# Kernel tuning notes

Hardware: AMD Instinct MI355X
Metric: run time of the kernel (lower is better)

## Reference

```python
import jax, jax.numpy as jnp
import numpy as np

B, QN, KN, DIN, DPROJ = 8, 2048, 2048, 1024, 1024

def setup_inputs() -> dict:
    key = jax.random.key(0)
    ks = jax.random.split(key, 10)
    s = 1.0 / np.sqrt(DIN)
    return {
        "query": jax.random.normal(ks[0], (B, QN, DIN), jnp.float32),
        "key": jax.random.normal(ks[1], (B, KN, DIN), jnp.float32),
        "value": jax.random.normal(ks[2], (B, KN, DIN), jnp.float32),
        "mask": jax.random.randint(ks[3], (B, KN), 0, 2, jnp.int32),
        "Wq": jax.random.uniform(ks[4], (DPROJ, DIN), jnp.float32, -s, s),
        "bq": jax.random.uniform(ks[5], (DPROJ,), jnp.float32, -s, s),
        "Wk": jax.random.uniform(ks[6], (DPROJ, DIN), jnp.float32, -s, s),
        "bk": jax.random.uniform(ks[7], (DPROJ,), jnp.float32, -s, s),
        "Wv": jax.random.uniform(ks[8], (DPROJ, DIN), jnp.float32, -s, s),
        "bv": jax.random.uniform(ks[9], (DPROJ,), jnp.float32, -s, s),
    }

def reference(query, key, value, mask, Wq, bq, Wk, bk, Wv, bv):
    pq = jnp.einsum('bqc,dc->bqd', query, Wq) + bq  # (b, qn, dproj)
    pk = jnp.einsum('bkc,dc->bkd', key, Wk) + bk    # (b, kn, dproj)
    pv = jnp.einsum('bkc,dc->bkd', value, Wv) + bv  # (b, kn, dproj)
    scores = jnp.einsum('bqd,bkd->bqk', pq, pk) / jnp.sqrt(jnp.float32(DPROJ))
    m = mask[:, None, :]  # (b, 1, kn) broadcasts over qn
    scores = jnp.where(m == 0, jnp.float32(-1e9), scores)
    attn = jax.nn.softmax(scores, axis=-1)
    attn = attn * m.astype(attn.dtype)  # post-softmax double mask
    ctx = jnp.einsum('bqk,bkd->bqd', attn, pv)
    return (ctx, attn)
```

## Files before the change

### kernel.cpp

```cpp
#include <hip/hip_runtime.h>
#include <hip/hip_bf16.h>


typedef __bf16 bf16;
typedef __bf16 bf16x4 __attribute__((ext_vector_type(4)));
typedef __bf16 bf16x8 __attribute__((ext_vector_type(8)));
typedef float f32x4 __attribute__((ext_vector_type(4)));

#define TILE 128
#define BK 32

__device__ __forceinline__ void gld_lds16(const bf16* g, bf16* l) {
  __builtin_amdgcn_global_load_lds(
      (const __attribute__((address_space(1))) void*)g,
      (__attribute__((address_space(3))) void*)l, 16, 0, 0);
}

__global__ __launch_bounds__(256, 2)
void gemm_f32in(const float* __restrict__ A, int lda,
                const float* __restrict__ Bt, int ldb,
                bf16* __restrict__ C, int ldc,
                const float* __restrict__ bias, int bias_mode, int K)
{
  __shared__ bf16 As[TILE * BK];
  __shared__ bf16 Bs[TILE * BK];
  const int tid = threadIdx.x;
  const int wave = tid >> 6, lane = tid & 63;
  const int wm = (wave >> 1) * 64, wn = (wave & 1) * 64;
  const long m0 = (long)blockIdx.x * TILE;
  const long n0 = (long)blockIdx.y * TILE;

  f32x4 acc[4][4] = {};
  const int fr = lane & 15, fq = lane >> 4;

  for (int k0 = 0; k0 < K; k0 += BK) {
    __syncthreads();
#pragma unroll
    for (int j = 0; j < 4; ++j) {
      int c = j * 256 + tid;
      int row = c >> 3, col = (c & 7) * 4;
      f32x4 av = *(const f32x4*)&A[(m0 + row) * (long)lda + k0 + col];
      f32x4 bv = *(const f32x4*)&Bt[(n0 + row) * (long)ldb + k0 + col];
      bf16x4 ab, bb;
      ab[0] = (bf16)av[0]; ab[1] = (bf16)av[1]; ab[2] = (bf16)av[2]; ab[3] = (bf16)av[3];
      bb[0] = (bf16)bv[0]; bb[1] = (bf16)bv[1]; bb[2] = (bf16)bv[2]; bb[3] = (bf16)bv[3];
      *(bf16x4*)&As[row * BK + col] = ab;
      *(bf16x4*)&Bs[row * BK + col] = bb;
    }
    __syncthreads();

    bf16x8 af[4], bg[4];
#pragma unroll
    for (int i = 0; i < 4; ++i)
      af[i] = *(const bf16x8*)&As[(wm + i * 16 + fr) * BK + fq * 8];
#pragma unroll
    for (int i = 0; i < 4; ++i)
      bg[i] = *(const bf16x8*)&Bs[(wn + i * 16 + fr) * BK + fq * 8];
#pragma unroll
    for (int mi = 0; mi < 4; ++mi)
#pragma unroll
      for (int ni = 0; ni < 4; ++ni)
        acc[mi][ni] = __builtin_amdgcn_mfma_f32_16x16x32_bf16(
            af[mi], bg[ni], acc[mi][ni], 0, 0, 0);
  }

  const int cc = lane & 15, cq = lane >> 4;
#pragma unroll
  for (int mi = 0; mi < 4; ++mi)
#pragma unroll
    for (int ni = 0; ni < 4; ++ni)
#pragma unroll
      for (int r = 0; r < 4; ++r) {
        int row = wm + mi * 16 + cq * 4 + r;
        int col = wn + ni * 16 + cc;
        float v = acc[mi][ni][r];
        if (bias_mode == 1) v += bias[n0 + col];
        else if (bias_mode == 2) v += bias[m0 + row];
        C[(m0 + row) * (long)ldc + (n0 + col)] = (bf16)v;
      }
}

__global__ __launch_bounds__(256, 2)
void gemm_bf16(const bf16* __restrict__ A, int lda, long sA,
               const bf16* __restrict__ Bt, int ldb, long sB,
               float* __restrict__ C, int ldc, long sC,
               int K, float scale)
{
  __shared__ bf16 As[TILE * BK];
  __shared__ bf16 Bs[TILE * BK];
  const int tid = threadIdx.x;
  const int wave = tid >> 6, lane = tid & 63;
  const int wm = (wave >> 1) * 64, wn = (wave & 1) * 64;
  const long m0 = (long)blockIdx.x * TILE;
  const long n0 = (long)blockIdx.y * TILE;
  A  += (long)blockIdx.z * sA;
  Bt += (long)blockIdx.z * sB;
  C  += (long)blockIdx.z * sC;

  f32x4 acc[4][4] = {};

  const int srow = tid >> 2;
  const int scol = (tid & 3) * 8;
  const bf16* Ag0 = A  + (m0 + srow) * (long)lda + scol;
  const bf16* Ag1 = A  + (m0 + 64 + srow) * (long)lda + scol;
  const bf16* Bg0 = Bt + (n0 + srow) * (long)ldb + scol;
  const bf16* Bg1 = Bt + (n0 + 64 + srow) * (long)ldb + scol;
  bf16* Al0 = &As[tid * 8];
  bf16* Al1 = &As[(256 + tid) * 8];
  bf16* Bl0 = &Bs[tid * 8];
  bf16* Bl1 = &Bs[(256 + tid) * 8];

  const int fr = lane & 15, fq = lane >> 4;

  for (int k0 = 0; k0 < K; k0 += BK) {
    __syncthreads();
    gld_lds16(Ag0 + k0, Al0);
    gld_lds16(Ag1 + k0, Al1);
    gld_lds16(Bg0 + k0, Bl0);
    gld_lds16(Bg1 + k0, Bl1);
    __syncthreads();

    bf16x8 af[4], bg[4];
#pragma unroll
    for (int i = 0; i < 4; ++i)
      af[i] = *(const bf16x8*)&As[(wm + i * 16 + fr) * BK + fq * 8];
#pragma unroll
    for (int i = 0; i < 4; ++i)
      bg[i] = *(const bf16x8*)&Bs[(wn + i * 16 + fr) * BK + fq * 8];
#pragma unroll
    for (int mi = 0; mi < 4; ++mi)
#pragma unroll
      for (int ni = 0; ni < 4; ++ni)
        acc[mi][ni] = __builtin_amdgcn_mfma_f32_16x16x32_bf16(
            af[mi], bg[ni], acc[mi][ni], 0, 0, 0);
  }

  const int cc = lane & 15, cq = lane >> 4;
#pragma unroll
  for (int mi = 0; mi < 4; ++mi)
#pragma unroll
    for (int ni = 0; ni < 4; ++ni)
#pragma unroll
      for (int r = 0; r < 4; ++r) {
        int row = wm + mi * 16 + cq * 4 + r;
        int col = wn + ni * 16 + cc;
        C[(m0 + row) * (long)ldc + (n0 + col)] = acc[mi][ni][r] * scale;
      }
}

__global__ __launch_bounds__(256)
void softmax_mask(const int* __restrict__ mask, float* __restrict__ attn,
                  bf16* __restrict__ attnb)
{
  const int row = blockIdx.x;
  const int b = row >> 11;
  float* arow = attn + (long)row * 2048;
  bf16* brow = attnb + (long)row * 2048;
  const int* mrow = mask + (b << 11);
  const int tid = threadIdx.x;
  const int lane = tid & 63, wave = tid >> 6;

  f32x4 s[2];
  int4 mk[2];
  s[0] = *(const f32x4*)&arow[tid * 4];
  s[1] = *(const f32x4*)&arow[1024 + tid * 4];
  mk[0] = *(const int4*)&mrow[tid * 4];
  mk[1] = *(const int4*)&mrow[1024 + tid * 4];
  const int m[8] = {mk[0].x, mk[0].y, mk[0].z, mk[0].w,
                    mk[1].x, mk[1].y, mk[1].z, mk[1].w};

  float mx = -3e38f;
#pragma unroll
  for (int i = 0; i < 8; ++i)
    if (m[i]) mx = fmaxf(mx, s[i >> 2][i & 3]);
#pragma unroll
  for (int off = 32; off > 0; off >>= 1) mx = fmaxf(mx, __shfl_xor(mx, off));
  __shared__ float rmax[4], rsum[4];
  if (lane == 0) rmax[wave] = mx;
  __syncthreads();
  mx = fmaxf(fmaxf(rmax[0], rmax[1]), fmaxf(rmax[2], rmax[3]));

  float e[8], sum = 0.f;
#pragma unroll
  for (int i = 0; i < 8; ++i) {
    e[i] = m[i] ? __expf(s[i >> 2][i & 3] - mx) : 0.f;
    sum += e[i];
  }
#pragma unroll
  for (int off = 32; off > 0; off >>= 1) sum += __shfl_xor(sum, off);
  if (lane == 0) rsum[wave] = sum;
  __syncthreads();
  sum = rsum[0] + rsum[1] + rsum[2] + rsum[3];
  float inv = sum > 0.f ? 1.f / sum : 0.f;

  f32x4 o; bf16x4 ob;
#pragma unroll
  for (int h = 0; h < 2; ++h) {
#pragma unroll
    for (int i = 0; i < 4; ++i) {
      float v = e[h * 4 + i] * inv;
      o[i] = v; ob[i] = (bf16)v;
    }
    *(f32x4*)&arow[h * 1024 + tid * 4] = o;
    *(bf16x4*)&brow[h * 1024 + tid * 4] = ob;
  }
}

extern "C" void kernel_launch(void* const* d_in, const int* in_sizes, int n_in,
                              void* d_out, int out_size, void* d_ws, size_t ws_size,
                              hipStream_t stream)
{
  const float* query = (const float*)d_in[0];
  const float* key   = (const float*)d_in[1];
  const float* value = (const float*)d_in[2];
  const int*   mask  = (const int*)d_in[3];
  const float* Wq = (const float*)d_in[4];
  const float* bq = (const float*)d_in[5];
  const float* Wk = (const float*)d_in[6];
  const float* bk = (const float*)d_in[7];
  const float* Wv = (const float*)d_in[8];
  const float* bv = (const float*)d_in[9];

  float* ctx  = (float*)d_out;
  float* attn = ctx + (size_t)8 * 2048 * 1024;

  bf16* Pq    = (bf16*)d_ws;
  bf16* Pk    = Pq + (size_t)16384 * 1024;
  bf16* PvT   = Pk + (size_t)16384 * 1024;
  bf16* attnb = (bf16*)d_ws;

  dim3 blk(256);

  hipLaunchKernelGGL(gemm_f32in, dim3(128, 8), blk, 0, stream,
      query, 1024, Wq, 1024, Pq, 1024, bq, 1, 1024);
  hipLaunchKernelGGL(gemm_f32in, dim3(128, 8), blk, 0, stream,
      key, 1024, Wk, 1024, Pk, 1024, bk, 1, 1024);
  hipLaunchKernelGGL(gemm_f32in, dim3(8, 128), blk, 0, stream,
      Wv, 1024, value, 1024, PvT, 16384, bv, 2, 1024);
  hipLaunchKernelGGL(gemm_bf16, dim3(16, 16, 8), blk, 0, stream,
      Pq, 1024, (long)2048 * 1024, Pk, 1024, (long)2048 * 1024,
      attn, 2048, (long)2048 * 2048, 1024, 0.03125f);
  hipLaunchKernelGGL(softmax_mask, dim3(16384), blk, 0, stream, mask, attn, attnb);
  hipLaunchKernelGGL(gemm_bf16, dim3(16, 8, 8), blk, 0, stream,
      attnb, 2048, (long)2048 * 2048, PvT, 16384, 2048L,
      ctx, 1024, (long)2048 * 1024, 2048, 1.0f);
}
```

Baseline: 766.0 us.

## Replace GEMMs with 256x256 8-wave pipelined kernel and pre-convert inputs to bf16

Adds a standalone f32-to-bf16 conversion pass for the inputs and weights, staged in the attn output buffer as scratch. All five GEMMs now use a new 512-thread kernel with 256x256 tiles, double-buffered LDS loaded through global_load_lds with XOR swizzle, split barriers and setprio. The score GEMM writes bf16 into the attn buffer, and softmax reads that bf16 data back, which halves score traffic at some cost in precision. The change brings more LDS use and extra conversion launches, and the intermediate scores now carry only bf16 precision.

```diff
diff --git a/kernel.cpp b/kernel.cpp
--- a/kernel.cpp
+++ b/kernel.cpp
@@ -7,8 +7,9 @@
 typedef __bf16 bf16x8 __attribute__((ext_vector_type(8)));
 typedef float f32x4 __attribute__((ext_vector_type(4)));
 
-#define TILE 128
-#define BK 32
+#define BAR() asm volatile("s_barrier" ::: "memory")
+#define WAIT_LGKM0() do { asm volatile("s_waitcnt lgkmcnt(0)" ::: "memory"); \
+                          __builtin_amdgcn_sched_barrier(0); } while (0)
 
 __device__ __forceinline__ void gld_lds16(const bf16* g, bf16* l) {
   __builtin_amdgcn_global_load_lds(
@@ -16,136 +17,201 @@
       (__attribute__((address_space(3))) void*)l, 16, 0, 0);
 }
 
-__global__ __launch_bounds__(256, 2)
-void gemm_f32in(const float* __restrict__ A, int lda,
-                const float* __restrict__ Bt, int ldb,
-                bf16* __restrict__ C, int ldc,
-                const float* __restrict__ bias, int bias_mode, int K)
+__global__ __launch_bounds__(256)
+void cvt_f32_bf16(const float* __restrict__ src, bf16* __restrict__ dst, int n)
 {
-  __shared__ bf16 As[TILE * BK];
-  __shared__ bf16 Bs[TILE * BK];
+  long i = ((long)blockIdx.x * 256 + threadIdx.x) * 8;
+  if (i >= n) return;
+  f32x4 a = *(const f32x4*)&src[i];
+  f32x4 b = *(const f32x4*)&src[i + 4];
+  bf16x8 o;
+  o[0] = (bf16)a[0]; o[1] = (bf16)a[1]; o[2] = (bf16)a[2]; o[3] = (bf16)a[3];
+  o[4] = (bf16)b[0]; o[5] = (bf16)b[1]; o[6] = (bf16)b[2]; o[7] = (bf16)b[3];
+  *(bf16x8*)&dst[i] = o;
+}
+
+__global__ __launch_bounds__(512, 2)
+void gemm8p(const bf16* __restrict__ A, int lda, long sA,
+            const bf16* __restrict__ Bt, int ldb, long sB,
+            void* __restrict__ Cout, int ldc, long sC, int c_bf16,
+            const float* __restrict__ bias, int bias_mode,
+            int K, float scale)
+{
+  extern __shared__ bf16 lds[];
   const int tid = threadIdx.x;
-  const int wave = tid >> 6, lane = tid & 63;
-  const int wm = (wave >> 1) * 64, wn = (wave & 1) * 64;
-  const long m0 = (long)blockIdx.x * TILE;
-  const long n0 = (long)blockIdx.y * TILE;
-
-  f32x4 acc[4][4] = {};
-  const int fr = lane & 15, fq = lane >> 4;
-
-  for (int k0 = 0; k0 < K; k0 += BK) {
-    __syncthreads();
-#pragma unroll
-    for (int j = 0; j < 4; ++j) {
-      int c = j * 256 + tid;
-      int row = c >> 3, col = (c & 7) * 4;
-      f32x4 av = *(const f32x4*)&A[(m0 + row) * (long)lda + k0 + col];
-      f32x4 bv = *(const f32x4*)&Bt[(n0 + row) * (long)ldb + k0 + col];
-      bf16x4 ab, bb;
-      ab[0] = (bf16)av[0]; ab[1] = (bf16)av[1]; ab[2] = (bf16)av[2]; ab[3] = (bf16)av[3];
-      bb[0] = (bf16)bv[0]; bb[1] = (bf16)bv[1]; bb[2] = (bf16)bv[2]; bb[3] = (bf16)bv[3];
-      *(bf16x4*)&As[row * BK + col] = ab;
-      *(bf16x4*)&Bs[row * BK + col] = bb;
-    }
-    __syncthreads();
-
-    bf16x8 af[4], bg[4];
-#pragma unroll
-    for (int i = 0; i < 4; ++i)
-      af[i] = *(const bf16x8*)&As[(wm + i * 16 + fr) * BK + fq * 8];
-#pragma unroll
-    for (int i = 0; i < 4; ++i)
-      bg[i] = *(const bf16x8*)&Bs[(wn + i * 16 + fr) * BK + fq * 8];
-#pragma unroll
-    for (int mi = 0; mi < 4; ++mi)
-#pragma unroll
-      for (int ni = 0; ni < 4; ++ni)
-        acc[mi][ni] = __builtin_amdgcn_mfma_f32_16x16x32_bf16(
-            af[mi], bg[ni], acc[mi][ni], 0, 0, 0);
-  }
-
-  const int cc = lane & 15, cq = lane >> 4;
-#pragma unroll
-  for (int mi = 0; mi < 4; ++mi)
-#pragma unroll
-    for (int ni = 0; ni < 4; ++ni)
-#pragma unroll
-      for (int r = 0; r < 4; ++r) {
-        int row = wm + mi * 16 + cq * 4 + r;
-        int col = wn + ni * 16 + cc;
-        float v = acc[mi][ni][r];
-        if (bias_mode == 1) v += bias[n0 + col];
-        else if (bias_mode == 2) v += bias[m0 + row];
-        C[(m0 + row) * (long)ldc + (n0 + col)] = (bf16)v;
-      }
-}
-
-__global__ __launch_bounds__(256, 2)
-void gemm_bf16(const bf16* __restrict__ A, int lda, long sA,
-               const bf16* __restrict__ Bt, int ldb, long sB,
-               float* __restrict__ C, int ldc, long sC,
-               int K, float scale)
-{
-  __shared__ bf16 As[TILE * BK];
-  __shared__ bf16 Bs[TILE * BK];
-  const int tid = threadIdx.x;
-  const int wave = tid >> 6, lane = tid & 63;
-  const int wm = (wave >> 1) * 64, wn = (wave & 1) * 64;
-  const long m0 = (long)blockIdx.x * TILE;
-  const long n0 = (long)blockIdx.y * TILE;
+  const int lane = tid & 63;
+  const int wid = tid >> 6;
+  const int wr = wid >> 2;
+  const int wc = wid & 3;
+  const long m0 = (long)blockIdx.x * 256;
+  const long n0 = (long)blockIdx.y * 256;
   A  += (long)blockIdx.z * sA;
   Bt += (long)blockIdx.z * sB;
-  C  += (long)blockIdx.z * sC;
-
-  f32x4 acc[4][4] = {};
-
-  const int srow = tid >> 2;
-  const int scol = (tid & 3) * 8;
-  const bf16* Ag0 = A  + (m0 + srow) * (long)lda + scol;
-  const bf16* Ag1 = A  + (m0 + 64 + srow) * (long)lda + scol;
-  const bf16* Bg0 = Bt + (n0 + srow) * (long)ldb + scol;
-  const bf16* Bg1 = Bt + (n0 + 64 + srow) * (long)ldb + scol;
-  bf16* Al0 = &As[tid * 8];
-  bf16* Al1 = &As[(256 + tid) * 8];
-  bf16* Bl0 = &Bs[tid * 8];
-  bf16* Bl1 = &Bs[(256 + tid) * 8];
 
   const int fr = lane & 15, fq = lane >> 4;
-
-  for (int k0 = 0; k0 < K; k0 += BK) {
-    __syncthreads();
-    gld_lds16(Ag0 + k0, Al0);
-    gld_lds16(Ag1 + k0, Al1);
-    gld_lds16(Bg0 + k0, Bl0);
-    gld_lds16(Bg1 + k0, Bl1);
-    __syncthreads();
-
-    bf16x8 af[4], bg[4];
-#pragma unroll
-    for (int i = 0; i < 4; ++i)
-      af[i] = *(const bf16x8*)&As[(wm + i * 16 + fr) * BK + fq * 8];
-#pragma unroll
-    for (int i = 0; i < 4; ++i)
-      bg[i] = *(const bf16x8*)&Bs[(wn + i * 16 + fr) * BK + fq * 8];
-#pragma unroll
-    for (int mi = 0; mi < 4; ++mi)
-#pragma unroll
-      for (int ni = 0; ni < 4; ++ni)
-        acc[mi][ni] = __builtin_amdgcn_mfma_f32_16x16x32_bf16(
-            af[mi], bg[ni], acc[mi][ni], 0, 0, 0);
+  const int cs0 = (((fq * 16)      ^ ((fr & 7) << 4)) >> 1);
+  const int cs1 = (((64 + fq * 16) ^ ((fr & 7) << 4)) >> 1);
+  const int rbA = (wr * 128 + fr) * 64;
+  const int rbB = 16384 + (wc * 64 + fr) * 64;
+
+  const int srow = tid >> 3;
+  const int slot = (tid & 7) ^ (srow & 7);
+  const bf16* Ag[4]; const bf16* Bg[4];
+#pragma unroll
+  for (int h = 0; h < 2; ++h)
+#pragma unroll
+    for (int i = 0; i < 2; ++i) {
+      Ag[h * 2 + i] = A  + (m0 + h * 128 + i * 64 + srow) * (long)lda + slot * 8;
+      Bg[h * 2 + i] = Bt + (n0 + h * 128 + i * 64 + srow) * (long)ldb + slot * 8;
+    }
+  const int ldst = tid * 8;
+
+  const int NT = K >> 6;
+  f32x4 acc[8][4] = {};
+
+#pragma unroll
+  for (int hi = 0; hi < 4; ++hi)
+    gld_lds16(Ag[hi], &lds[(hi >> 1) * 8192 + (hi & 1) * 4096 + ldst]);
+#pragma unroll
+  for (int hi = 0; hi < 4; ++hi)
+    gld_lds16(Bg[hi], &lds[16384 + (hi >> 1) * 8192 + (hi & 1) * 4096 + ldst]);
+#pragma unroll
+  for (int hi = 0; hi < 4; ++hi)
+    gld_lds16(Bg[hi] + 64, &lds[49152 + (hi >> 1) * 8192 + (hi & 1) * 4096 + ldst]);
+  asm volatile("s_waitcnt vmcnt(4)" ::: "memory");
+  BAR();
+
+  for (int t = 0; t < NT; ++t) {
+    const int bo  = (t & 1) << 15;
+    const int nbo = bo ^ 32768;
+    const int kof  = (t + 1) * 64;
+    const int kof2 = (t + 2) * 64;
+    const bool st1 = (t + 1 < NT), st2 = (t + 2 < NT);
+
+    bf16x8 a0[4][2], b0[2][2], b1[2][2];
+
+#pragma unroll
+    for (int mf = 0; mf < 4; ++mf) {
+      a0[mf][0] = *(const bf16x8*)&lds[bo + rbA + mf * 1024 + cs0];
+      a0[mf][1] = *(const bf16x8*)&lds[bo + rbA + mf * 1024 + cs1];
+    }
+#pragma unroll
+    for (int nf = 0; nf < 2; ++nf) {
+      b0[nf][0] = *(const bf16x8*)&lds[bo + rbB + nf * 1024 + cs0];
+      b0[nf][1] = *(const bf16x8*)&lds[bo + rbB + nf * 1024 + cs1];
+    }
+    if (st1) {
+      gld_lds16(Ag[0] + kof, &lds[nbo + ldst]);
+      gld_lds16(Ag[1] + kof, &lds[nbo + 4096 + ldst]);
+    }
+    BAR(); WAIT_LGKM0();
+    __builtin_amdgcn_s_setprio(1);
+#pragma unroll
+    for (int mf = 0; mf < 4; ++mf)
+#pragma unroll
+      for (int nf = 0; nf < 2; ++nf) {
+        acc[mf][nf] = __builtin_amdgcn_mfma_f32_16x16x32_bf16(a0[mf][0], b0[nf][0], acc[mf][nf], 0, 0, 0);
+        acc[mf][nf] = __builtin_amdgcn_mfma_f32_16x16x32_bf16(a0[mf][1], b0[nf][1], acc[mf][nf], 0, 0, 0);
+      }
+    __builtin_amdgcn_s_setprio(0);
+    BAR();
+
+#pragma unroll
+    for (int nf = 0; nf < 2; ++nf) {
+      b1[nf][0] = *(const bf16x8*)&lds[bo + rbB + (nf + 2) * 1024 + cs0];
+      b1[nf][1] = *(const bf16x8*)&lds[bo + rbB + (nf + 2) * 1024 + cs1];
+    }
+    if (st1) {
+      gld_lds16(Ag[2] + kof, &lds[nbo + 8192 + ldst]);
+      gld_lds16(Ag[3] + kof, &lds[nbo + 8192 + 4096 + ldst]);
+    }
+    BAR(); WAIT_LGKM0();
+    __builtin_amdgcn_s_setprio(1);
+#pragma unroll
+    for (int mf = 0; mf < 4; ++mf)
+#pragma unroll
+      for (int nf = 0; nf < 2; ++nf) {
+        acc[mf][nf + 2] = __builtin_amdgcn_mfma_f32_16x16x32_bf16(a0[mf][0], b1[nf][0], acc[mf][nf + 2], 0, 0, 0);
+        acc[mf][nf + 2] = __builtin_amdgcn_mfma_f32_16x16x32_bf16(a0[mf][1], b1[nf][1], acc[mf][nf + 2], 0, 0, 0);
+      }
+    __builtin_amdgcn_s_setprio(0);
+    BAR();
+
+#pragma unroll
+    for (int mf = 0; mf < 4; ++mf) {
+      a0[mf][0] = *(const bf16x8*)&lds[bo + rbA + (mf + 4) * 1024 + cs0];
+      a0[mf][1] = *(const bf16x8*)&lds[bo + rbA + (mf + 4) * 1024 + cs1];
+    }
+    if (st2) {
+      gld_lds16(Bg[0] + kof2, &lds[bo + 16384 + ldst]);
+      gld_lds16(Bg[1] + kof2, &lds[bo + 16384 + 4096 + ldst]);
+    }
+    BAR(); WAIT_LGKM0();
+    __builtin_amdgcn_s_setprio(1);
+#pragma unroll
+    for (int mf = 0; mf < 4; ++mf)
+#pragma unroll
+      for (int nf = 0; nf < 2; ++nf) {
+        acc[mf + 4][nf + 2] = __builtin_amdgcn_mfma_f32_16x16x32_bf16(a0[mf][0], b1[nf][0], acc[mf + 4][nf + 2], 0, 0, 0);
+        acc[mf + 4][nf + 2] = __builtin_amdgcn_mfma_f32_16x16x32_bf16(a0[mf][1], b1[nf][1], acc[mf + 4][nf + 2], 0, 0, 0);
+      }
+    __builtin_amdgcn_s_setprio(0);
+    BAR();
+
+    if (st2) {
+      gld_lds16(Bg[2] + kof2, &lds[bo + 16384 + 8192 + ldst]);
+      gld_lds16(Bg[3] + kof2, &lds[bo + 16384 + 8192 + 4096 + ldst]);
+      asm volatile("s_waitcnt vmcnt(4)" ::: "memory");
+    } else {
+      asm volatile("s_waitcnt vmcnt(0)" ::: "memory");
+    }
+    BAR(); WAIT_LGKM0();
+    __builtin_amdgcn_s_setprio(1);
+#pragma unroll
+    for (int mf = 0; mf < 4; ++mf)
+#pragma unroll
+      for (int nf = 0; nf < 2; ++nf) {
+        acc[mf + 4][nf] = __builtin_amdgcn_mfma_f32_16x16x32_bf16(a0[mf][0], b0[nf][0], acc[mf + 4][nf], 0, 0, 0);
+        acc[mf + 4][nf] = __builtin_amdgcn_mfma_f32_16x16x32_bf16(a0[mf][1], b0[nf][1], acc[mf + 4][nf], 0, 0, 0);
+      }
+    __builtin_amdgcn_s_setprio(0);
+    BAR();
   }
 
   const int cc = lane & 15, cq = lane >> 4;
-#pragma unroll
-  for (int mi = 0; mi < 4; ++mi)
-#pragma unroll
-    for (int ni = 0; ni < 4; ++ni)
-#pragma unroll
-      for (int r = 0; r < 4; ++r) {
-        int row = wm + mi * 16 + cq * 4 + r;
-        int col = wn + ni * 16 + cc;
-        C[(m0 + row) * (long)ldc + (n0 + col)] = acc[mi][ni][r] * scale;
-      }
+  const long crow0 = m0 + wr * 128;
+  const long ccol0 = n0 + wc * 64;
+  if (c_bf16) {
+    bf16* C = (bf16*)Cout + (long)blockIdx.z * sC;
+#pragma unroll
+    for (int mf = 0; mf < 8; ++mf)
+#pragma unroll
+      for (int nf = 0; nf < 4; ++nf)
+#pragma unroll
+        for (int r = 0; r < 4; ++r) {
+          long row = crow0 + mf * 16 + cq * 4 + r;
+          long col = ccol0 + nf * 16 + cc;
+          float v = acc[mf][nf][r] * scale;
+          if (bias_mode == 1) v += bias[col];
+          else if (bias_mode == 2) v += bias[row];
+          C[row * (long)ldc + col] = (bf16)v;
+        }
+  } else {
+    float* C = (float*)Cout + (long)blockIdx.z * sC;
+#pragma unroll
+    for (int mf = 0; mf < 8; ++mf)
+#pragma unroll
+      for (int nf = 0; nf < 4; ++nf)
+#pragma unroll
+        for (int r = 0; r < 4; ++r) {
+          long row = crow0 + mf * 16 + cq * 4 + r;
+          long col = ccol0 + nf * 16 + cc;
+          float v = acc[mf][nf][r] * scale;
+          if (bias_mode == 1) v += bias[col];
+          else if (bias_mode == 2) v += bias[row];
+          C[row * (long)ldc + col] = v;
+        }
+  }
 }
 
 __global__ __launch_bounds__(256)
@@ -155,24 +221,28 @@
   const int row = blockIdx.x;
   const int b = row >> 11;
   float* arow = attn + (long)row * 2048;
+  const bf16* srow_b = (const bf16*)arow;
   bf16* brow = attnb + (long)row * 2048;
   const int* mrow = mask + (b << 11);
   const int tid = threadIdx.x;
   const int lane = tid & 63, wave = tid >> 6;
 
-  f32x4 s[2];
+  bf16x4 sb[2];
   int4 mk[2];
-  s[0] = *(const f32x4*)&arow[tid * 4];
-  s[1] = *(const f32x4*)&arow[1024 + tid * 4];
+  sb[0] = *(const bf16x4*)&srow_b[tid * 4];
+  sb[1] = *(const bf16x4*)&srow_b[1024 + tid * 4];
   mk[0] = *(const int4*)&mrow[tid * 4];
   mk[1] = *(const int4*)&mrow[1024 + tid * 4];
   const int m[8] = {mk[0].x, mk[0].y, mk[0].z, mk[0].w,
                     mk[1].x, mk[1].y, mk[1].z, mk[1].w};
+  float s[8];
+#pragma unroll
+  for (int i = 0; i < 8; ++i) s[i] = (float)sb[i >> 2][i & 3];
 
   float mx = -3e38f;
 #pragma unroll
   for (int i = 0; i < 8; ++i)
-    if (m[i]) mx = fmaxf(mx, s[i >> 2][i & 3]);
+    if (m[i]) mx = fmaxf(mx, s[i]);
 #pragma unroll
   for (int off = 32; off > 0; off >>= 1) mx = fmaxf(mx, __shfl_xor(mx, off));
   __shared__ float rmax[4], rsum[4];
@@ -183,7 +253,7 @@
   float e[8], sum = 0.f;
 #pragma unroll
   for (int i = 0; i < 8; ++i) {
-    e[i] = m[i] ? __expf(s[i >> 2][i & 3] - mx) : 0.f;
+    e[i] = m[i] ? __expf(s[i] - mx) : 0.f;
     sum += e[i];
   }
 #pragma unroll
@@ -229,19 +299,40 @@
   bf16* PvT   = Pk + (size_t)16384 * 1024;
   bf16* attnb = (bf16*)d_ws;
 
-  dim3 blk(256);
-
-  hipLaunchKernelGGL(gemm_f32in, dim3(128, 8), blk, 0, stream,
-      query, 1024, Wq, 1024, Pq, 1024, bq, 1, 1024);
-  hipLaunchKernelGGL(gemm_f32in, dim3(128, 8), blk, 0, stream,
-      key, 1024, Wk, 1024, Pk, 1024, bk, 1, 1024);
-  hipLaunchKernelGGL(gemm_f32in, dim3(8, 128), blk, 0, stream,
-      Wv, 1024, value, 1024, PvT, 16384, bv, 2, 1024);
-  hipLaunchKernelGGL(gemm_bf16, dim3(16, 16, 8), blk, 0, stream,
+  bf16* qb  = (bf16*)attn;
+  bf16* kb  = qb + (size_t)16384 * 1024;
+  bf16* vb  = kb + (size_t)16384 * 1024;
+  bf16* Wqb = vb + (size_t)16384 * 1024;
+  bf16* Wkb = Wqb + (size_t)1024 * 1024;
+  bf16* Wvb = Wkb + (size_t)1024 * 1024;
+
+  static bool attr_set = false;
+  if (!attr_set) {
+    hipFuncSetAttribute(reinterpret_cast<const void*>(gemm8p),
+                        hipFuncAttributeMaxDynamicSharedMemorySize, 131072);
+    attr_set = true;
+  }
+
+  dim3 blk(256), blk8(512);
+
+  hipLaunchKernelGGL(cvt_f32_bf16, dim3(8192), blk, 0, stream, query, qb, 16384 * 1024);
+  hipLaunchKernelGGL(cvt_f32_bf16, dim3(8192), blk, 0, stream, key,   kb, 16384 * 1024);
+  hipLaunchKernelGGL(cvt_f32_bf16, dim3(8192), blk, 0, stream, value, vb, 16384 * 1024);
+  hipLaunchKernelGGL(cvt_f32_bf16, dim3(512),  blk, 0, stream, Wq, Wqb, 1024 * 1024);
+  hipLaunchKernelGGL(cvt_f32_bf16, dim3(512),  blk, 0, stream, Wk, Wkb, 1024 * 1024);
+  hipLaunchKernelGGL(cvt_f32_bf16, dim3(512),  blk, 0, stream, Wv, Wvb, 1024 * 1024);
+
+  hipLaunchKernelGGL(gemm8p, dim3(64, 4, 1), blk8, 131072, stream,
+      qb, 1024, 0L, Wqb, 1024, 0L, (void*)Pq, 1024, 0L, 1, bq, 1, 1024, 1.0f);
+  hipLaunchKernelGGL(gemm8p, dim3(64, 4, 1), blk8, 131072, stream,
+      kb, 1024, 0L, Wkb, 1024, 0L, (void*)Pk, 1024, 0L, 1, bk, 1, 1024, 1.0f);
+  hipLaunchKernelGGL(gemm8p, dim3(4, 64, 1), blk8, 131072, stream,
+      Wvb, 1024, 0L, vb, 1024, 0L, (void*)PvT, 16384, 0L, 1, bv, 2, 1024, 1.0f);
+  hipLaunchKernelGGL(gemm8p, dim3(8, 8, 8), blk8, 131072, stream,
       Pq, 1024, (long)2048 * 1024, Pk, 1024, (long)2048 * 1024,
-      attn, 2048, (long)2048 * 2048, 1024, 0.03125f);
+      (void*)attn, 4096, (long)2048 * 4096, 1, (const float*)nullptr, 0, 1024, 0.03125f);
   hipLaunchKernelGGL(softmax_mask, dim3(16384), blk, 0, stream, mask, attn, attnb);
-  hipLaunchKernelGGL(gemm_bf16, dim3(16, 8, 8), blk, 0, stream,
+  hipLaunchKernelGGL(gemm8p, dim3(8, 4, 8), blk8, 131072, stream,
       attnb, 2048, (long)2048 * 2048, PvT, 16384, 2048L,
-      ctx, 1024, (long)2048 * 1024, 2048, 1.0f);
-}
+      (void*)ctx, 1024, (long)2048 * 1024, 0, (const float*)nullptr, 0, 2048, 1.0f);
+}
```

New measurement: 681.7 us. -11.0%, faster.
